# Kernel optimization log

Hardware: AMD Instinct MI355X
Metric: run time of the kernel (lower is better)

## Reference

```python
import jax, jax.numpy as jnp
import numpy as np
from jax import lax

B, T_IN, D = 32, 512, 384
F = 384      # x_predictor_filter_size
K = 3        # kernel, padding=1 -> same length
LN_EPS = 1e-5


def setup_inputs() -> dict:
    key = jax.random.key(0)
    ks = jax.random.split(key, 8)
    s = 0.02
    return {
        "x": jax.random.normal(ks[0], (B, T_IN, D), dtype=jnp.float32),
        "target": jax.random.randint(ks[1], (B, T_IN), 0, 8, dtype=jnp.int32),
        "mel_max_length": 4096,
        "conv1_w": jax.random.normal(ks[2], (F, D, K), dtype=jnp.float32) * s,
        "conv1_b": jnp.zeros((F,), jnp.float32),
        "ln1_g": jnp.ones((F,), jnp.float32),
        "ln1_b": jnp.zeros((F,), jnp.float32),
        "conv2_w": jax.random.normal(ks[3], (F, F, K), dtype=jnp.float32) * s,
        "conv2_b": jnp.zeros((F,), jnp.float32),
        "ln2_g": jnp.ones((F,), jnp.float32),
        "ln2_b": jnp.zeros((F,), jnp.float32),
        "lin_w": jax.random.normal(ks[4], (F, 1), dtype=jnp.float32) * s,
        "lin_b": jnp.zeros((1,), jnp.float32),
    }


def _conv1d_same(h_ncl, w, b):
    # h_ncl: [B, C_in, T], w: [C_out, C_in, K], padding=1
    out = lax.conv_general_dilated(h_ncl, w, window_strides=(1,), padding=[(1, 1)],
                                   dimension_numbers=("NCH", "OIH", "NCH"))
    return out + b[None, :, None]


def _layernorm(h, g, b):
    mu = jnp.mean(h, axis=-1, keepdims=True)
    var = jnp.var(h, axis=-1, keepdims=True)
    return (h - mu) * lax.rsqrt(var + LN_EPS) * g + b


def _duration_predictor(x, conv1_w, conv1_b, ln1_g, ln1_b, conv2_w, conv2_b, ln2_g, ln2_b, lin_w, lin_b):
    h = _conv1d_same(jnp.transpose(x, (0, 2, 1)), conv1_w, conv1_b)       # [B,F,T]
    h = jax.nn.relu(_layernorm(jnp.transpose(h, (0, 2, 1)), ln1_g, ln1_b))  # [B,T,F]
    h = _conv1d_same(jnp.transpose(h, (0, 2, 1)), conv2_w, conv2_b)
    h = jax.nn.relu(_layernorm(jnp.transpose(h, (0, 2, 1)), ln2_g, ln2_b))
    return (h @ lin_w + lin_b)[..., 0]  # [B, T_in]


def _length_regulate(x, target, mel_max_length):
    # Equivalent to alignment @ x with one-hot alignment built by create_alignment,
    # expressed as a duration-indexed gather (same math, no dense [B,Tout,Tin]).
    ends = jnp.cumsum(target, axis=1)                 # [B, T_in]
    m = jnp.arange(mel_max_length)                    # [T_out]
    idx = jax.vmap(lambda e: jnp.searchsorted(e, m, side="right"))(ends)  # [B, T_out]
    valid = idx < target.shape[1]                     # frames past total duration -> zero pad
    idx = jnp.minimum(idx, target.shape[1] - 1)
    out = jnp.take_along_axis(x, idx[:, :, None], axis=1)  # [B, T_out, D]
    return out * valid[:, :, None].astype(x.dtype)


def reference(x, target, mel_max_length, conv1_w, conv1_b, ln1_g, ln1_b,
              conv2_w, conv2_b, ln2_g, ln2_b, lin_w, lin_b):
    dur_pred = _duration_predictor(x, conv1_w, conv1_b, ln1_g, ln1_b,
                                   conv2_w, conv2_b, ln2_g, ln2_b, lin_w, lin_b)
    output = _length_regulate(x, target, mel_max_length)
    return output, dur_pred
```

## Files before the change

### kernel.cpp

```cpp
#include <hip/hip_runtime.h>
#include <cstdint>
#include <cstddef>

#define B_   32
#define TIN  512
#define D_   384
#define F_   384
#define TOUT 4096
#define TPAD 514
#define MTOT (B_ * TIN)

typedef __bf16 bf16x8 __attribute__((ext_vector_type(8)));
typedef float  f32x4  __attribute__((ext_vector_type(4)));

__device__ __forceinline__ unsigned short f2bf(float f) {
  unsigned int u = __float_as_uint(f);
  u += 0x7fff + ((u >> 16) & 1);
  return (unsigned short)(u >> 16);
}

__device__ __forceinline__ void load16_to_lds(const void* g, void* l) {
  __builtin_amdgcn_global_load_lds(
      (const __attribute__((address_space(1))) unsigned int*)g,
      (__attribute__((address_space(3))) unsigned int*)l, 16, 0, 0);
}

#define PB_CUM 32
#define PB_W   3456
#define PB_Z   96
#define PB_PX  6168
#define PB_TOT (PB_CUM + PB_W + PB_Z + PB_PX)

__global__ __launch_bounds__(256) void prep_all(
    const float* __restrict__ w1, const float* __restrict__ w2,
    unsigned short* __restrict__ Wt1, unsigned short* __restrict__ Wt2,
    unsigned short* __restrict__ h1p,
    const int* __restrict__ target, int* __restrict__ idxv,
    const float4* __restrict__ x4, unsigned short* __restrict__ xp) {
  int bx = blockIdx.x;
  int tid = threadIdx.x;

  if (bx < PB_CUM) {
    __shared__ int ends[512];
    __shared__ int ps[256];
    int b = bx;
    int a0 = target[b * TIN + 2 * tid];
    int a1 = target[b * TIN + 2 * tid + 1];
    ps[tid] = a0 + a1;
    __syncthreads();
    for (int off = 1; off < 256; off <<= 1) {
      int add = (tid >= off) ? ps[tid - off] : 0;
      __syncthreads();
      ps[tid] += add;
      __syncthreads();
    }
    int incl = ps[tid];
    ends[2 * tid + 1] = incl;
    ends[2 * tid]     = incl - a1;
    __syncthreads();
    for (int p = 0; p < 16; ++p) {
      int m = p * 256 + tid;
      int lo = 0, hi = 512;
      while (lo < hi) {
        int mid = (lo + hi) >> 1;
        if (ends[mid] <= m) lo = mid + 1; else hi = mid;
      }
      idxv[b * TOUT + m] = (lo < TIN) ? lo : -1;
    }
    return;
  }
  bx -= PB_CUM;

  if (bx < PB_W) {
    int g = bx * 256 + tid;
    const int WE = 3 * F_ * D_;
    int which = g >= WE;
    const float* w = which ? w2 : w1;
    unsigned short* o = which ? Wt2 : Wt1;
    int e = g - which * WE;
    int k = e / (F_ * D_);
    int rem = e - k * (F_ * D_);
    int f = rem / D_;
    int d = rem - f * D_;
    o[e] = f2bf(w[(f * D_ + d) * 3 + k]);
    return;
  }
  bx -= PB_W;

  if (bx < PB_Z) {
    int z = bx * 256 + tid;
    int zr = z / D_;
    int c = z - zr * D_;
    int b = zr >> 1;
    int tp = (zr & 1) ? (TPAD - 1) : 0;
    h1p[((size_t)(b * TPAD + tp)) * D_ + c] = 0;
    return;
  }
  bx -= PB_Z;

  {
    int g = bx * 256 + tid;
    int row = g / 96;
    int c4 = g - row * 96;
    int b = row / TPAD;
    int tp = row - b * TPAD;
    ushort4 o;
    if (tp == 0 || tp == TPAD - 1) {
      o.x = 0; o.y = 0; o.z = 0; o.w = 0;
    } else {
      float4 v = x4[((size_t)(b * TIN + tp - 1)) * 96 + c4];
      o.x = f2bf(v.x); o.y = f2bf(v.y); o.z = f2bf(v.z); o.w = f2bf(v.w);
    }
    *(ushort4*)(xp + (size_t)row * D_ + c4 * 4) = o;
  }
}

__device__ __forceinline__ void conv_tile(const unsigned short* __restrict__ Ap,
                                          const unsigned short* __restrict__ Wt,
                                          const float* __restrict__ bias,
                                          float* __restrict__ out, int cb) {
  __shared__ __align__(16) unsigned short As[128 * 32];
  __shared__ __align__(16) unsigned short Bs[128 * 32];
  const int tid  = threadIdx.x;
  const int wave = tid >> 6;
  const int lane = tid & 63;
  const int quad = lane >> 4;
  const int l15  = lane & 15;
  const int wm = (wave >> 1) * 64;
  const int wn = (wave & 1) * 64;
  const int mt = cb / 3;
  const int nt = cb - mt * 3;
  const int m0 = mt * 128;
  const int n0 = nt * 128;
  const int b  = m0 >> 9;
  const int t0 = m0 & 511;

  const int srow = tid >> 2;
  const int scol = (tid & 3) * 8;

  f32x4 acc[4][4];
  for (int i = 0; i < 4; ++i)
    for (int j = 0; j < 4; ++j)
      acc[i][j] = (f32x4){0.f, 0.f, 0.f, 0.f};

  for (int kc = 0; kc < 36; ++kc) {
    int kw = kc / 12;
    int d0 = (kc - kw * 12) * 32;
    for (int r = 0; r < 2; ++r) {
      int row = r * 64 + srow;
      const unsigned short* ga = Ap + (size_t)(b * TPAD + t0 + row + kw) * D_ + d0 + scol;
      load16_to_lds(ga, (char*)As + r * 4096 + wave * 1024);
      const unsigned short* gb = Wt + (size_t)(kw * F_ + n0 + row) * D_ + d0 + scol;
      load16_to_lds(gb, (char*)Bs + r * 4096 + wave * 1024);
    }
    __syncthreads();
    bf16x8 av[4], bv[4];
    for (int mi = 0; mi < 4; ++mi)
      av[mi] = *(const bf16x8*)(As + (wm + mi * 16 + l15) * 32 + quad * 8);
    for (int ni = 0; ni < 4; ++ni)
      bv[ni] = *(const bf16x8*)(Bs + (wn + ni * 16 + l15) * 32 + quad * 8);
    for (int mi = 0; mi < 4; ++mi)
      for (int ni = 0; ni < 4; ++ni)
        acc[mi][ni] = __builtin_amdgcn_mfma_f32_16x16x32_bf16(av[mi], bv[ni], acc[mi][ni], 0, 0, 0);
    __syncthreads();
  }

  for (int mi = 0; mi < 4; ++mi) {
    int mrow = m0 + wm + mi * 16 + quad * 4;
    for (int ni = 0; ni < 4; ++ni) {
      int ncol = n0 + wn + ni * 16 + l15;
      float bb = bias[ncol];
      for (int r = 0; r < 4; ++r)
        out[(size_t)(mrow + r) * F_ + ncol] = acc[mi][ni][r] + bb;
    }
  }
}

__global__ __launch_bounds__(256) void conv_gather(
    const unsigned short* __restrict__ Ap, const unsigned short* __restrict__ Wt,
    const float* __restrict__ bias, float* __restrict__ out,
    const float4* __restrict__ x4, const int* __restrict__ idxv,
    float4* __restrict__ out4, int gpart) {
  int bx = blockIdx.x;
  if ((bx & 1) == 0) {
    conv_tile(Ap, Wt, bias, out, bx >> 1);
  } else {
    int gb = gpart * 384 + (bx >> 1);
    int g = gb * 256 + (int)threadIdx.x;
    for (int it = 0; it < 64; ++it, g += 768 * 256) {
      int fr = g / 96;
      int c = g - fr * 96;
      int id = idxv[fr];
      int b = fr >> 12;
      float4 v = {0.f, 0.f, 0.f, 0.f};
      if (id >= 0) v = x4[(size_t)(b * TIN + id) * 96 + c];
      out4[g] = v;
    }
  }
}

__global__ void ln_relu(const float* __restrict__ in, const float* __restrict__ gam,
                        const float* __restrict__ bet, unsigned short* __restrict__ hp) {
  int row = blockIdx.x * 4 + (threadIdx.x >> 6);
  int lane = threadIdx.x & 63;
  const float* p = in + (size_t)row * F_;
  float v[6];
  float s = 0.f, ss = 0.f;
  for (int j = 0; j < 6; ++j) {
    v[j] = p[lane + j * 64];
    s += v[j];
    ss += v[j] * v[j];
  }
  for (int off = 32; off; off >>= 1) {
    s  += __shfl_xor(s, off);
    ss += __shfl_xor(ss, off);
  }
  float mean = s * (1.f / 384.f);
  float var  = ss * (1.f / 384.f) - mean * mean;
  float rstd = rsqrtf(var + 1e-5f);
  int b = row >> 9, t = row & 511;
  unsigned short* o = hp + ((size_t)(b * TPAD + t + 1)) * D_;
  for (int j = 0; j < 6; ++j) {
    int c = lane + j * 64;
    float y = (v[j] - mean) * rstd * gam[c] + bet[c];
    y = y > 0.f ? y : 0.f;
    o[c] = f2bf(y);
  }
}

__global__ void ln_dot(const float* __restrict__ in, const float* __restrict__ gam,
                       const float* __restrict__ bet, const float* __restrict__ lw,
                       const float* __restrict__ lb, float* __restrict__ dur) {
  int row = blockIdx.x * 4 + (threadIdx.x >> 6);
  int lane = threadIdx.x & 63;
  const float* p = in + (size_t)row * F_;
  float v[6];
  float s = 0.f, ss = 0.f;
  for (int j = 0; j < 6; ++j) {
    v[j] = p[lane + j * 64];
    s += v[j];
    ss += v[j] * v[j];
  }
  for (int off = 32; off; off >>= 1) {
    s  += __shfl_xor(s, off);
    ss += __shfl_xor(ss, off);
  }
  float mean = s * (1.f / 384.f);
  float var  = ss * (1.f / 384.f) - mean * mean;
  float rstd = rsqrtf(var + 1e-5f);
  float acc = 0.f;
  for (int j = 0; j < 6; ++j) {
    int c = lane + j * 64;
    float y = (v[j] - mean) * rstd * gam[c] + bet[c];
    y = y > 0.f ? y : 0.f;
    acc += y * lw[c];
  }
  for (int off = 32; off; off >>= 1) acc += __shfl_xor(acc, off);
  if (lane == 0) dur[row] = acc + lb[0];
}

extern "C" void kernel_launch(void* const* d_in, const int* in_sizes, int n_in,
                              void* d_out, int out_size, void* d_ws, size_t ws_size,
                              hipStream_t stream) {
  const float* x      = (const float*)d_in[0];
  const int*   target = (const int*)d_in[1];
  const float* w1  = (const float*)d_in[3];
  const float* b1  = (const float*)d_in[4];
  const float* g1  = (const float*)d_in[5];
  const float* be1 = (const float*)d_in[6];
  const float* w2  = (const float*)d_in[7];
  const float* b2  = (const float*)d_in[8];
  const float* g2  = (const float*)d_in[9];
  const float* be2 = (const float*)d_in[10];
  const float* lw  = (const float*)d_in[11];
  const float* lb  = (const float*)d_in[12];

  float* out = (float*)d_out;
  float* dur = out + (size_t)B_ * TOUT * D_;

  char* ws = (char*)d_ws;
  unsigned short* xp  = (unsigned short*)(ws);
  unsigned short* h1p = (unsigned short*)(ws + 12632064);
  unsigned short* Wt1 = (unsigned short*)(ws + 25264128);
  unsigned short* Wt2 = (unsigned short*)(ws + 26148864);
  float*          gbf = (float*)(ws + 27033600);
  int*            idxv = (int*)(ws + 52199424);

  hipLaunchKernelGGL(prep_all, dim3(PB_TOT), dim3(256), 0, stream,
                     w1, w2, Wt1, Wt2, h1p, target, idxv, (const float4*)x, xp);
  hipLaunchKernelGGL(conv_gather, dim3(768), dim3(256), 0, stream,
                     xp, Wt1, b1, gbf, (const float4*)x, idxv, (float4*)out, 0);
  hipLaunchKernelGGL(ln_relu, dim3(4096), dim3(256), 0, stream, gbf, g1, be1, h1p);
  hipLaunchKernelGGL(conv_gather, dim3(768), dim3(256), 0, stream,
                     h1p, Wt2, b2, gbf, (const float4*)x, idxv, (float4*)out, 1);
  hipLaunchKernelGGL(ln_dot, dim3(4096), dim3(256), 0, stream, gbf, g2, be2, lw, lb, dur);
}
```

Before: 321.7 us.

## Fuse LayerNorm epilogue into conv GEMM with full-width tiles and interleaved gather

Each conv block now computes a 128x384 output tile with 512 threads, so the full channel row is available in LDS. LayerNorm, ReLU and either the bf16 store or the final dot product run in the epilogue. This removes the separate ln_relu and ln_dot kernels and the fp32 intermediate round trip. Gather work is still interleaved, now at 4 gather blocks per conv block. The trade-offs are larger LDS and register use per block and fewer conv blocks (128) for the GPU to spread across.

Measured after the change: 554.9 us. 72.5% more time.

```diff
diff --git a/kernel.cpp b/kernel.cpp
--- a/kernel.cpp
+++ b/kernel.cpp
@@ -115,148 +115,139 @@
   }
 }
 
-__device__ __forceinline__ void conv_tile(const unsigned short* __restrict__ Ap,
-                                          const unsigned short* __restrict__ Wt,
-                                          const float* __restrict__ bias,
-                                          float* __restrict__ out, int cb) {
-  __shared__ __align__(16) unsigned short As[128 * 32];
-  __shared__ __align__(16) unsigned short Bs[128 * 32];
-  const int tid  = threadIdx.x;
+template <int MODE>
+__global__ __launch_bounds__(512, 2) void conv_fused(
+    const unsigned short* __restrict__ Ap, const unsigned short* __restrict__ Wt,
+    const float* __restrict__ bias,
+    const float* __restrict__ gam, const float* __restrict__ bet,
+    const float* __restrict__ lw, const float* __restrict__ lb,
+    unsigned short* __restrict__ hp, float* __restrict__ dur,
+    const float4* __restrict__ x4, const int* __restrict__ idxv,
+    float4* __restrict__ out4, int half) {
+  __shared__ __align__(16) char smem[49152];
+  unsigned short* As = (unsigned short*)smem;
+  unsigned short* Bs = (unsigned short*)(smem + 8192);
+  float* epi = (float*)smem;
+
+  const int bx  = blockIdx.x;
+  const int tid = threadIdx.x;
+  const int cbq = bx / 5;
+
+  if (bx - cbq * 5 != 0) {
+    int gidx = bx - cbq - 1;
+    size_t g = (size_t)half * 6291456 + (size_t)gidx * 512 + tid;
+    for (int it = 0; it < 24; ++it, g += 262144) {
+      unsigned int gu = (unsigned int)g;
+      int fr = gu / 96;
+      int c  = gu - fr * 96;
+      int id = idxv[fr];
+      int b  = fr >> 12;
+      float4 v = {0.f, 0.f, 0.f, 0.f};
+      if (id >= 0) v = x4[(size_t)(b * TIN + id) * 96 + c];
+      out4[g] = v;
+    }
+    return;
+  }
+
   const int wave = tid >> 6;
   const int lane = tid & 63;
   const int quad = lane >> 4;
   const int l15  = lane & 15;
-  const int wm = (wave >> 1) * 64;
-  const int wn = (wave & 1) * 64;
-  const int mt = cb / 3;
-  const int nt = cb - mt * 3;
-  const int m0 = mt * 128;
-  const int n0 = nt * 128;
+  const int wr = wave >> 2;
+  const int wc = wave & 3;
+  const int wm = wr * 64;
+  const int wn = wc * 96;
+  const int m0 = cbq * 128;
   const int b  = m0 >> 9;
   const int t0 = m0 & 511;
-
-  const int srow = tid >> 2;
-  const int scol = (tid & 3) * 8;
-
-  f32x4 acc[4][4];
+  const int arow = tid >> 2;
+  const int acol = (tid & 3) * 8;
+
+  f32x4 acc[4][6];
   for (int i = 0; i < 4; ++i)
-    for (int j = 0; j < 4; ++j)
+    for (int j = 0; j < 6; ++j)
       acc[i][j] = (f32x4){0.f, 0.f, 0.f, 0.f};
 
   for (int kc = 0; kc < 36; ++kc) {
     int kw = kc / 12;
     int d0 = (kc - kw * 12) * 32;
-    for (int r = 0; r < 2; ++r) {
-      int row = r * 64 + srow;
-      const unsigned short* ga = Ap + (size_t)(b * TPAD + t0 + row + kw) * D_ + d0 + scol;
-      load16_to_lds(ga, (char*)As + r * 4096 + wave * 1024);
-      const unsigned short* gb = Wt + (size_t)(kw * F_ + n0 + row) * D_ + d0 + scol;
-      load16_to_lds(gb, (char*)Bs + r * 4096 + wave * 1024);
-    }
-    __syncthreads();
-    bf16x8 av[4], bv[4];
+    load16_to_lds(Ap + (size_t)(b * TPAD + t0 + arow + kw) * D_ + d0 + acol,
+                  (char*)As + tid * 16);
+    for (int r = 0; r < 3; ++r)
+      load16_to_lds(Wt + (size_t)(kw * F_ + r * 128 + arow) * D_ + d0 + acol,
+                    (char*)Bs + r * 8192 + tid * 16);
+    __syncthreads();
+    bf16x8 av[4], bv[6];
     for (int mi = 0; mi < 4; ++mi)
       av[mi] = *(const bf16x8*)(As + (wm + mi * 16 + l15) * 32 + quad * 8);
-    for (int ni = 0; ni < 4; ++ni)
+    for (int ni = 0; ni < 6; ++ni)
       bv[ni] = *(const bf16x8*)(Bs + (wn + ni * 16 + l15) * 32 + quad * 8);
     for (int mi = 0; mi < 4; ++mi)
-      for (int ni = 0; ni < 4; ++ni)
+      for (int ni = 0; ni < 6; ++ni)
         acc[mi][ni] = __builtin_amdgcn_mfma_f32_16x16x32_bf16(av[mi], bv[ni], acc[mi][ni], 0, 0, 0);
     __syncthreads();
   }
 
-  for (int mi = 0; mi < 4; ++mi) {
-    int mrow = m0 + wm + mi * 16 + quad * 4;
-    for (int ni = 0; ni < 4; ++ni) {
-      int ncol = n0 + wn + ni * 16 + l15;
-      float bb = bias[ncol];
-      for (int r = 0; r < 4; ++r)
-        out[(size_t)(mrow + r) * F_ + ncol] = acc[mi][ni][r] + bb;
-    }
-  }
-}
-
-__global__ __launch_bounds__(256) void conv_gather(
-    const unsigned short* __restrict__ Ap, const unsigned short* __restrict__ Wt,
-    const float* __restrict__ bias, float* __restrict__ out,
-    const float4* __restrict__ x4, const int* __restrict__ idxv,
-    float4* __restrict__ out4, int gpart) {
-  int bx = blockIdx.x;
-  if ((bx & 1) == 0) {
-    conv_tile(Ap, Wt, bias, out, bx >> 1);
-  } else {
-    int gb = gpart * 384 + (bx >> 1);
-    int g = gb * 256 + (int)threadIdx.x;
-    for (int it = 0; it < 64; ++it, g += 768 * 256) {
-      int fr = g / 96;
-      int c = g - fr * 96;
-      int id = idxv[fr];
-      int b = fr >> 12;
-      float4 v = {0.f, 0.f, 0.f, 0.f};
-      if (id >= 0) v = x4[(size_t)(b * TIN + id) * 96 + c];
-      out4[g] = v;
-    }
-  }
-}
-
-__global__ void ln_relu(const float* __restrict__ in, const float* __restrict__ gam,
-                        const float* __restrict__ bet, unsigned short* __restrict__ hp) {
-  int row = blockIdx.x * 4 + (threadIdx.x >> 6);
-  int lane = threadIdx.x & 63;
-  const float* p = in + (size_t)row * F_;
-  float v[6];
-  float s = 0.f, ss = 0.f;
-  for (int j = 0; j < 6; ++j) {
-    v[j] = p[lane + j * 64];
-    s += v[j];
-    ss += v[j] * v[j];
-  }
-  for (int off = 32; off; off >>= 1) {
-    s  += __shfl_xor(s, off);
-    ss += __shfl_xor(ss, off);
-  }
-  float mean = s * (1.f / 384.f);
-  float var  = ss * (1.f / 384.f) - mean * mean;
-  float rstd = rsqrtf(var + 1e-5f);
-  int b = row >> 9, t = row & 511;
-  unsigned short* o = hp + ((size_t)(b * TPAD + t + 1)) * D_;
+  float bse[6], gv[6], bv2[6], lwv[6];
   for (int j = 0; j < 6; ++j) {
     int c = lane + j * 64;
-    float y = (v[j] - mean) * rstd * gam[c] + bet[c];
-    y = y > 0.f ? y : 0.f;
-    o[c] = f2bf(y);
-  }
-}
-
-__global__ void ln_dot(const float* __restrict__ in, const float* __restrict__ gam,
-                       const float* __restrict__ bet, const float* __restrict__ lw,
-                       const float* __restrict__ lb, float* __restrict__ dur) {
-  int row = blockIdx.x * 4 + (threadIdx.x >> 6);
-  int lane = threadIdx.x & 63;
-  const float* p = in + (size_t)row * F_;
-  float v[6];
-  float s = 0.f, ss = 0.f;
-  for (int j = 0; j < 6; ++j) {
-    v[j] = p[lane + j * 64];
-    s += v[j];
-    ss += v[j] * v[j];
-  }
-  for (int off = 32; off; off >>= 1) {
-    s  += __shfl_xor(s, off);
-    ss += __shfl_xor(ss, off);
-  }
-  float mean = s * (1.f / 384.f);
-  float var  = ss * (1.f / 384.f) - mean * mean;
-  float rstd = rsqrtf(var + 1e-5f);
-  float acc = 0.f;
-  for (int j = 0; j < 6; ++j) {
-    int c = lane + j * 64;
-    float y = (v[j] - mean) * rstd * gam[c] + bet[c];
-    y = y > 0.f ? y : 0.f;
-    acc += y * lw[c];
-  }
-  for (int off = 32; off; off >>= 1) acc += __shfl_xor(acc, off);
-  if (lane == 0) dur[row] = acc + lb[0];
+    gv[j]  = gam[c];
+    bv2[j] = bet[c];
+    if (MODE == 1) lwv[j] = lw[c];
+  }
+  float bb[6];
+  for (int ni = 0; ni < 6; ++ni) bb[ni] = bias[wn + ni * 16 + l15];
+
+  for (int g4 = 0; g4 < 4; ++g4) {
+    __syncthreads();
+    if (wr == (g4 >> 1)) {
+      for (int mh = 0; mh < 2; ++mh) {
+        int mi = (g4 & 1) * 2 + mh;
+        int lrb = mh * 16 + quad * 4;
+        for (int ni = 0; ni < 6; ++ni) {
+          int c = wn + ni * 16 + l15;
+          for (int r = 0; r < 4; ++r)
+            epi[(lrb + r) * 384 + c] = acc[mi][ni][r] + bb[ni];
+        }
+      }
+    }
+    __syncthreads();
+    for (int rr = 0; rr < 4; ++rr) {
+      int lr = wave * 4 + rr;
+      int grow = m0 + g4 * 32 + lr;
+      const float* p = epi + lr * 384;
+      float v[6], s = 0.f, ss = 0.f;
+      for (int j = 0; j < 6; ++j) {
+        v[j] = p[lane + j * 64];
+        s += v[j];
+        ss += v[j] * v[j];
+      }
+      for (int off = 32; off; off >>= 1) {
+        s  += __shfl_xor(s, off);
+        ss += __shfl_xor(ss, off);
+      }
+      float mean = s * (1.f / 384.f);
+      float var  = ss * (1.f / 384.f) - mean * mean;
+      float rstd = rsqrtf(var + 1e-5f);
+      if (MODE == 0) {
+        unsigned short* o = hp + ((size_t)(b * TPAD + (grow & 511) + 1)) * D_;
+        for (int j = 0; j < 6; ++j) {
+          float y = (v[j] - mean) * rstd * gv[j] + bv2[j];
+          y = y > 0.f ? y : 0.f;
+          o[lane + j * 64] = f2bf(y);
+        }
+      } else {
+        float a = 0.f;
+        for (int j = 0; j < 6; ++j) {
+          float y = (v[j] - mean) * rstd * gv[j] + bv2[j];
+          y = y > 0.f ? y : 0.f;
+          a += y * lwv[j];
+        }
+        for (int off = 32; off; off >>= 1) a += __shfl_xor(a, off);
+        if (lane == 0) dur[grow] = a + lb[0];
+      }
+    }
+  }
 }
 
 extern "C" void kernel_launch(void* const* d_in, const int* in_sizes, int n_in,
@@ -279,19 +270,18 @@
   float* dur = out + (size_t)B_ * TOUT * D_;
 
   char* ws = (char*)d_ws;
-  unsigned short* xp  = (unsigned short*)(ws);
-  unsigned short* h1p = (unsigned short*)(ws + 12632064);
-  unsigned short* Wt1 = (unsigned short*)(ws + 25264128);
-  unsigned short* Wt2 = (unsigned short*)(ws + 26148864);
-  float*          gbf = (float*)(ws + 27033600);
-  int*            idxv = (int*)(ws + 52199424);
-
-  hipLaunchKernelGGL(prep_all, dim3(PB_TOT), dim3(256), 0, stream,
-                     w1, w2, Wt1, Wt2, h1p, target, idxv, (const float4*)x, xp);
-  hipLaunchKernelGGL(conv_gather, dim3(768), dim3(256), 0, stream,
-                     xp, Wt1, b1, gbf, (const float4*)x, idxv, (float4*)out, 0);
-  hipLaunchKernelGGL(ln_relu, dim3(4096), dim3(256), 0, stream, gbf, g1, be1, h1p);
-  hipLaunchKernelGGL(conv_gather, dim3(768), dim3(256), 0, stream,
-                     h1p, Wt2, b2, gbf, (const float4*)x, idxv, (float4*)out, 1);
-  hipLaunchKernelGGL(ln_dot, dim3(4096), dim3(256), 0, stream, gbf, g2, be2, lw, lb, dur);
-}
+  unsigned short* xp   = (unsigned short*)(ws);
+  unsigned short* h1p  = (unsigned short*)(ws + 12632064);
+  unsigned short* Wt1  = (unsigned short*)(ws + 25264128);
+  unsigned short* Wt2  = (unsigned short*)(ws + 26148864);
+  int*            idxv = (int*)(ws + 27033600);
+
+  prep_all<<<dim3(PB_TOT), dim3(256), 0, stream>>>(
+      w1, w2, Wt1, Wt2, h1p, target, idxv, (const float4*)x, xp);
+  conv_fused<0><<<dim3(640), dim3(512), 0, stream>>>(
+      xp, Wt1, b1, g1, be1, nullptr, nullptr, h1p, nullptr,
+      (const float4*)x, idxv, (float4*)out, 0);
+  conv_fused<1><<<dim3(640), dim3(512), 0, stream>>>(
+      h1p, Wt2, b2, g2, be2, lw, lb, nullptr, dur,
+      (const float4*)x, idxv, (float4*)out, 1);
+}
```
